# Kernel tuning notes

Hardware: AMD Instinct MI355X
Metric: run time of the kernel (lower is better)

The kernel has to match this reference:

```python
import jax, jax.numpy as jnp
import numpy as np

N, E, IN, HID, OUT = 50000, 800000, 128, 64, 32
ALPHA, BETA, DIVIDER = 0.5, 0.5, 5.0


def _gcn_conv(x, edge_index, W, b, alpha=ALPHA, beta=BETA):
    """DirectedGCNConv.forward: add self loops, linear, degree-normalized gather-mul-scatter."""
    n = x.shape[0]
    loops = jnp.arange(n, dtype=edge_index.dtype)
    row = jnp.concatenate([edge_index[0], loops])  # sources
    col = jnp.concatenate([edge_index[1], loops])  # targets
    x = x @ W.T + b                                # [n, out]
    ones = jnp.ones(row.shape[0], dtype=x.dtype)
    in_deg = jax.ops.segment_sum(ones, col, num_segments=n)
    out_deg = jax.ops.segment_sum(ones, row, num_segments=n)
    norm = in_deg[col] ** (-alpha) * out_deg[row] ** (-beta)  # [E+n]
    msgs = norm[:, None] * x[row]                  # gather + scale
    return jax.ops.segment_sum(msgs, col, num_segments=n)  # scatter-add aggr


def _source_enc(x, ei, W1, b1, W2, b2):
    x = jax.nn.relu(_gcn_conv(x, ei, W1, b1))
    return _gcn_conv(x, jnp.flip(ei, axis=0), W2, b2)


def _target_enc(x, ei, W1, b1, W2, b2):
    x = jax.nn.relu(_gcn_conv(x, jnp.flip(ei, axis=0), W1, b1))
    return _gcn_conv(x, ei, W2, b2)


def setup_inputs() -> dict:
    key = jax.random.key(0)
    ks = jax.random.split(key, 24)

    def lin(kw, kb, o, i, scale):
        return (jax.random.normal(kw, (o, i), jnp.float32) * scale,
                jax.random.normal(kb, (o,), jnp.float32) * 0.01)

    s1 = (2.0 / (IN + HID)) ** 0.5
    s2 = (2.0 / (HID + OUT)) ** 0.5
    inp = {
        "s": jax.random.normal(ks[0], (N, IN), jnp.float32),
        "t": jax.random.normal(ks[1], (N, IN), jnp.float32),
        "edge_index": jax.random.randint(ks[2], (2, E), 0, N, jnp.int32),
        "noise_s": jax.random.normal(ks[3], (N, OUT), jnp.float32),
        "noise_t": jax.random.normal(ks[4], (N, OUT), jnp.float32),
    }
    names = ["sm", "sl", "tm", "tl"]  # source/target mu/logstd encoders
    k = 5
    for nm in names:
        W1, b1 = lin(ks[k], ks[k + 1], HID, IN, s1); k += 2
        W2, b2 = lin(ks[k], ks[k + 1], OUT, HID, s2); k += 2
        inp[nm + "1_W"], inp[nm + "1_b"] = W1, b1
        inp[nm + "2_W"], inp[nm + "2_b"] = W2, b2
    return inp


def reference(s, t, edge_index, noise_s, noise_t,
              sm1_W, sm1_b, sm2_W, sm2_b,
              sl1_W, sl1_b, sl2_W, sl2_b,
              tm1_W, tm1_b, tm2_W, tm2_b,
              tl1_W, tl1_b, tl2_W, tl2_b):
    s_mu = _source_enc(s, edge_index, sm1_W, sm1_b, sm2_W, sm2_b)
    s_logstd = _source_enc(s, edge_index, sl1_W, sl1_b, sl2_W, sl2_b)
    t_mu = _target_enc(t, edge_index, tm1_W, tm1_b, tm2_W, tm2_b)
    t_logstd = _target_enc(t, edge_index, tl1_W, tl1_b, tl2_W, tl2_b)
    # reparametrize_edges (training mode), noise materialized as input
    s_out = s_mu + noise_s * jnp.exp(s_logstd) / DIVIDER
    t_out = t_mu + noise_t * jnp.exp(t_logstd) / DIVIDER
    return (s_out, t_out)
```

## Files before the change

### kernel.cpp

```cpp
#include <hip/hip_runtime.h>
#include <hip/hip_fp16.h>
#include <math.h>

#define N_NODES 50000
#define NPACK 25000
#define E_EDGES 800000
#define NCHUNKS ((N_NODES + 1023) / 1024)
#define LIN_BLOCKS 1564
#define QCH 64
#define CHUNK (E_EDGES / QCH)
#define CHUNK4 (CHUNK / 4)
#define OCT_NODES 12500
#define OCT_PACK 6250
#define HIST_BLOCKS 512
#define HL_GRID (HIST_BLOCKS + LIN_BLOCKS)
#define FOCT_NODES 6250
#define FOCT_PACK 3125
#define FILL_BLOCKS 1024
#define LCAP 4096

typedef _Float16 half8 __attribute__((ext_vector_type(8)));
typedef float f32x4 __attribute__((ext_vector_type(4)));

__device__ inline float fac_from(unsigned int u) {
    unsigned short us = (unsigned short)(u >> 16);
    __half h;
    __builtin_memcpy(&h, &us, 2);
    return __half2float(h);
}

__device__ inline int unpack_cnt(const unsigned int* cntp, int i) {
    unsigned int w = cntp[i >> 1];
    return (i & 1) ? (int)(w >> 16) : (int)(w & 0xffff);
}

__global__ __launch_bounds__(256) void w2h_kernel(const float* __restrict__ sW2a,
                                                  const float* __restrict__ sW2b,
                                                  const float* __restrict__ tW2a,
                                                  const float* __restrict__ tW2b,
                                                  const float* __restrict__ sW1a,
                                                  const float* __restrict__ sW1b,
                                                  const float* __restrict__ tW1a,
                                                  const float* __restrict__ tW1b,
                                                  __half* __restrict__ hw2,
                                                  __half* __restrict__ hw1) {
    int i = blockIdx.x * 256 + threadIdx.x;
    if (i < 4 * 2048) {
        const float* s2[4] = { sW2a, sW2b, tW2a, tW2b };
        hw2[i] = __float2half(s2[i >> 11][i & 2047]);
        return;
    }
    int j = i - 4 * 2048;
    if (j < 4 * 8192) {
        const float* s1[4] = { sW1a, sW1b, tW1a, tW1b };
        hw1[j] = __float2half(s1[j >> 13][j & 8191]);
    }
}

__global__ __launch_bounds__(256) void hist_lin1_kernel(const int* __restrict__ ei0,
                                                        const int* __restrict__ ei1,
                                                        unsigned int* __restrict__ ghist,
                                                        unsigned short* __restrict__ list,
                                                        unsigned int* __restrict__ cnt_bkt,
                                                        const float* __restrict__ Xs,
                                                        const float* __restrict__ Xt,
                                                        const __half* __restrict__ hw1,
                                                        const float* __restrict__ sba,
                                                        const float* __restrict__ sbb,
                                                        const float* __restrict__ tba,
                                                        const float* __restrict__ tbb,
                                                        __half* __restrict__ As,
                                                        __half* __restrict__ At, int n) {
    __shared__ unsigned int h[OCT_PACK];
    __shared__ unsigned int lcnt;
    int bx = blockIdx.x;
    int tid = threadIdx.x;
    if (bx < HIST_BLOCKS) {
        int oct = bx & 3, q = (bx >> 2) & 63, dir = bx >> 8;
        for (int i = tid; i < OCT_PACK; i += 256) h[i] = 0;
        if (tid == 0) lcnt = 0;
        __syncthreads();
        const int* key = dir ? ei0 : ei1;
        const uint4* key4 = (const uint4*)(key + q * CHUNK);
        unsigned short* lst = list + ((size_t)(dir * QCH + q) * 4 + oct) * LCAP;
        int lo = oct * OCT_NODES;
        for (int j = tid; j < CHUNK4; j += 256) {
            uint4 k4 = key4[j];
            int vv[4] = { (int)k4.x, (int)k4.y, (int)k4.z, (int)k4.w };
#pragma unroll
            for (int e = 0; e < 4; ++e) {
                unsigned int d = (unsigned int)(vv[e] - lo);
                if (d < OCT_NODES) {
                    atomicAdd(&h[d >> 1], 1u << ((d & 1) * 16));
                    unsigned int slot = atomicAdd(&lcnt, 1u);
                    if (slot < LCAP) lst[slot] = (unsigned short)(j * 4 + e);
                }
            }
        }
        __syncthreads();
        unsigned int* g = ghist + (size_t)(dir * QCH + q) * NPACK + oct * OCT_PACK;
        for (int i = tid; i < OCT_PACK; i += 256) g[i] = h[i];
        if (tid == 0) cnt_bkt[dir * 256 + q * 4 + oct] = (lcnt < LCAP) ? lcnt : LCAP;
        return;
    }
    int lidx = bx - HIST_BLOCKS;
    int y = lidx & 1;
    int xb = lidx >> 1;
    const float* X = y ? Xt : Xs;
    const __half* Wset[2] = { hw1 + (size_t)(y * 2 + 0) * 8192,
                              hw1 + (size_t)(y * 2 + 1) * 8192 };
    const float* bset[2] = { y ? tba : sba, y ? tbb : sbb };
    __half* A = y ? At : As;

    int w = tid >> 6, lane = tid & 63;
    int quad = lane >> 4, col = lane & 15;
    int node0 = xb * 64 + w * 16;

    half8 afrag[4];
    {
        int row = node0 + col;
        if (row >= n) row = n - 1;
        const float* xr = X + (size_t)row * 128 + quad * 8;
#pragma unroll
        for (int kc = 0; kc < 4; ++kc) {
            float4 f0 = *(const float4*)(xr + kc * 32);
            float4 f1 = *(const float4*)(xr + kc * 32 + 4);
            half8 hh;
            hh[0] = (_Float16)f0.x; hh[1] = (_Float16)f0.y;
            hh[2] = (_Float16)f0.z; hh[3] = (_Float16)f0.w;
            hh[4] = (_Float16)f1.x; hh[5] = (_Float16)f1.y;
            hh[6] = (_Float16)f1.z; hh[7] = (_Float16)f1.w;
            afrag[kc] = hh;
        }
    }

#pragma unroll
    for (int set = 0; set < 2; ++set) {
        const __half* Ws = Wset[set] + (size_t)0;
#pragma unroll
        for (int nt = 0; nt < 4; ++nt) {
            float bb = bset[set][nt * 16 + col];
            f32x4 acc = { bb, bb, bb, bb };
            const __half* wr = Ws + (size_t)(nt * 16 + col) * 128 + quad * 8;
#pragma unroll
            for (int kc = 0; kc < 4; ++kc) {
                half8 bfr = *(const half8*)(wr + kc * 32);
                acc = __builtin_amdgcn_mfma_f32_16x16x32_f16(afrag[kc], bfr, acc, 0, 0, 0);
            }
#pragma unroll
            for (int r = 0; r < 4; ++r) {
                int node = node0 + quad * 4 + r;
                if (node < n)
                    A[(size_t)node * 128 + set * 64 + nt * 16 + col] = __float2half(acc[r]);
            }
        }
    }
}

__global__ __launch_bounds__(256) void nodescan_kernel(unsigned int* __restrict__ ghist,
                                                       unsigned int* __restrict__ cntp) {
    int vp = blockIdx.x * 256 + threadIdx.x;
    int dir = blockIdx.y;
    if (vp >= NPACK) return;
    unsigned int lo = 0, hi = 0;
    unsigned int* g = ghist + (size_t)dir * QCH * NPACK + vp;
#pragma unroll 4
    for (int q = 0; q < QCH; ++q) {
        unsigned int w = g[(size_t)q * NPACK];
        g[(size_t)q * NPACK] = lo | (hi << 16);
        lo += w & 0xffff;
        hi += w >> 16;
    }
    cntp[dir * NPACK + vp] = lo | (hi << 16);
}

__global__ __launch_bounds__(1024) void scan_chunk2_kernel(const unsigned int* __restrict__ cntp,
                                                           int* __restrict__ offs_f,
                                                           int* __restrict__ offs_b,
                                                           int* __restrict__ part_f,
                                                           int* __restrict__ part_b, int n) {
    const unsigned int* cnt = cntp + (blockIdx.y ? NPACK : 0);
    int* offs = blockIdx.y ? offs_b : offs_f;
    int* partials = blockIdx.y ? part_b : part_f;
    __shared__ int sh[1024];
    int tid = threadIdx.x;
    int i = blockIdx.x * 1024 + tid;
    int v = (i < n) ? unpack_cnt(cnt, i) : 0;
    sh[tid] = v;
    __syncthreads();
    for (int off = 1; off < 1024; off <<= 1) {
        int add = (tid >= off) ? sh[tid - off] : 0;
        __syncthreads();
        sh[tid] += add;
        __syncthreads();
    }
    if (i < n) offs[i] = sh[tid] - v;
    if (tid == 1023) partials[blockIdx.x] = sh[tid];
}

__global__ __launch_bounds__(256) void addback_deg_kernel(int* __restrict__ offs_f,
                                                          int* __restrict__ offs_b,
                                                          const int* __restrict__ part_f,
                                                          const int* __restrict__ part_b,
                                                          const unsigned int* __restrict__ cntp,
                                                          float* dsi, float* dti,
                                                          unsigned short* __restrict__ h_dsi,
                                                          unsigned short* __restrict__ h_dti,
                                                          int n, int nchunks) {
    __shared__ int sp[64];
    int tid = threadIdx.x;
    const int* part = blockIdx.y ? part_b : part_f;
    if (tid < 64) sp[tid] = (tid < nchunks) ? part[tid] : 0;
    __syncthreads();
    if (tid == 0) {
        int run = 0;
        for (int k = 0; k < 64; ++k) { int t = sp[k]; sp[k] = run; run += t; }
    }
    __syncthreads();
    int i = blockIdx.x * 256 + tid;
    if (blockIdx.y == 0) {
        if (i < n) {
            offs_f[i] += sp[i >> 10];
            float f = rsqrtf((float)(unpack_cnt(cntp, i) + 1));
            dti[i] = f;
            __half hf = __float2half(f);
            unsigned short hb; __builtin_memcpy(&hb, &hf, 2);
            h_dti[i] = hb;
        } else if (i == n) offs_f[n] = sp[nchunks];
    } else {
        if (i < n) {
            offs_b[i] += sp[i >> 10];
            float f = rsqrtf((float)(unpack_cnt(cntp + NPACK, i) + 1));
            dsi[i] = f;
            __half hf = __float2half(f);
            unsigned short hb; __builtin_memcpy(&hb, &hf, 2);
            h_dsi[i] = hb;
        } else if (i == n) offs_b[n] = sp[nchunks];
    }
}

__global__ __launch_bounds__(256) void fill_kernel(const int* __restrict__ ei0,
                                                   const int* __restrict__ ei1,
                                                   const unsigned int* __restrict__ ghist,
                                                   const int* __restrict__ offs_f,
                                                   const int* __restrict__ offs_b,
                                                   const unsigned short* __restrict__ h_dsi,
                                                   const unsigned short* __restrict__ h_dti,
                                                   unsigned int* __restrict__ pay_f,
                                                   unsigned int* __restrict__ pay_b,
                                                   const unsigned short* __restrict__ list,
                                                   const unsigned int* __restrict__ cnt_bkt) {
    __shared__ unsigned int pos[FOCT_NODES];
    int bx = blockIdx.x;
    int foct = bx & 7, q = (bx >> 3) & 63, dir = bx >> 9;
    int oct = foct >> 1;
    int tid = threadIdx.x;
    const unsigned int* pref = ghist + (size_t)(dir * QCH + q) * NPACK + foct * FOCT_PACK;
    const int* offs = dir ? offs_b : offs_f;
    int lo = foct * FOCT_NODES;
    for (int d = tid; d < FOCT_NODES; d += 256) {
        unsigned int pw = pref[d >> 1];
        int cb = (d & 1) ? (int)(pw >> 16) : (int)(pw & 0xffff);
        pos[d] = (unsigned int)(offs[lo + d] + cb);
    }
    __syncthreads();
    const int* key = dir ? ei0 : ei1;
    const int* pid = dir ? ei1 : ei0;
    const unsigned short* hfac = dir ? h_dti : h_dsi;
    unsigned int* pay = dir ? pay_b : pay_f;
    const unsigned short* lst = list + ((size_t)(dir * QCH + q) * 4 + oct) * LCAP;
    int cnt = (int)cnt_bkt[dir * 256 + q * 4 + oct];
    int base = q * CHUNK;
    for (int j = tid; j < cnt; j += 256) {
        int gi = base + (int)lst[j];
        int v = key[gi];
        unsigned int d = (unsigned int)(v - lo);
        if (d < FOCT_NODES) {
            int id = pid[gi];
            unsigned int p = atomicAdd(&pos[d], 1u);
            unsigned int hb = hfac[id];
            pay[p] = (unsigned int)id | (hb << 16);
        }
    }
}

__device__ inline void acc_fma(float* acc, uint4 u, float f) {
    const __half2* h = (const __half2*)&u;
    float2 f0 = __half22float2(h[0]);
    float2 f1 = __half22float2(h[1]);
    float2 f2 = __half22float2(h[2]);
    float2 f3 = __half22float2(h[3]);
    acc[0] += f * f0.x; acc[1] += f * f0.y; acc[2] += f * f1.x; acc[3] += f * f1.y;
    acc[4] += f * f2.x; acc[5] += f * f2.y; acc[6] += f * f3.x; acc[7] += f * f3.y;
}

__global__ __launch_bounds__(256) void pull_lin2_kernel(const __half* __restrict__ As,
                                                        const __half* __restrict__ At,
                                                        __half* __restrict__ Cs,
                                                        __half* __restrict__ Ct,
                                                        const int* __restrict__ offs_f,
                                                        const int* __restrict__ offs_b,
                                                        const unsigned int* __restrict__ pay_f,
                                                        const unsigned int* __restrict__ pay_b,
                                                        const float* __restrict__ dsi,
                                                        const float* __restrict__ dti,
                                                        const float* __restrict__ sb2a,
                                                        const float* __restrict__ sb2b,
                                                        const float* __restrict__ tb2a,
                                                        const float* __restrict__ tb2b,
                                                        const __half* __restrict__ hw2, int n) {
    int y = blockIdx.y;
    const __half* xw = y ? At : As;
    __half* C = y ? Ct : Cs;
    const int* offs = y ? offs_b : offs_f;
    const unsigned int* pay = y ? pay_b : pay_f;
    const float* fac_self  = y ? dsi : dti;
    const float* fac_other = y ? dti : dsi;
    const float* b2a = y ? tb2a : sb2a;
    const float* b2b = y ? tb2b : sb2b;

    __shared__ __half xsh[16 * 136];

    int tid = threadIdx.x;
    int ln = tid >> 4;
    int f4 = tid & 15;
    int v = blockIdx.x * 16 + ln;
    int i = offs[v], end = offs[v + 1];
    const uint4* xw16 = (const uint4*)xw;

    float acc[8] = {0, 0, 0, 0, 0, 0, 0, 0};
    acc_fma(acc, xw16[v * 16 + f4], fac_other[v]);
    while (i < end && (i & 3)) {
        unsigned int pk = pay[i];
        acc_fma(acc, xw16[(pk & 0xffff) * 16 + f4], fac_from(pk));
        ++i;
    }
    for (; i + 3 < end; i += 4) {
        uint4 pk = *(const uint4*)(pay + i);
        int s0 = pk.x & 0xffff, s1 = pk.y & 0xffff;
        int s2 = pk.z & 0xffff, s3 = pk.w & 0xffff;
        uint4 ua = xw16[s0 * 16 + f4];
        uint4 ub = xw16[s1 * 16 + f4];
        uint4 uc = xw16[s2 * 16 + f4];
        uint4 ud = xw16[s3 * 16 + f4];
        acc_fma(acc, ua, fac_from(pk.x));
        acc_fma(acc, ub, fac_from(pk.y));
        acc_fma(acc, uc, fac_from(pk.z));
        acc_fma(acc, ud, fac_from(pk.w));
    }
    for (; i < end; ++i) {
        unsigned int pk = pay[i];
        acc_fma(acc, xw16[(pk & 0xffff) * 16 + f4], fac_from(pk));
    }

    float fs = fac_self[v];
    half8 hx;
#pragma unroll
    for (int j = 0; j < 8; ++j) hx[j] = (_Float16)fmaxf(acc[j] * fs, 0.0f);
    *(half8*)&xsh[ln * 136 + f4 * 8] = hx;
    __syncthreads();

    int w = tid >> 6, lane = tid & 63;
    int s = w >> 1, nt = w & 1;
    int quad = lane >> 4, col = lane & 15;
    float bb = (s ? b2b : b2a)[nt * 16 + col];
    f32x4 cacc = { bb, bb, bb, bb };
    const __half* hw = hw2 + (size_t)(y * 2 + s) * 2048;
#pragma unroll
    for (int t = 0; t < 2; ++t) {
        half8 af = *(const half8*)&xsh[col * 136 + s * 64 + t * 32 + quad * 8];
        half8 bf = *(const half8*)&hw[(nt * 16 + col) * 64 + t * 32 + quad * 8];
        cacc = __builtin_amdgcn_mfma_f32_16x16x32_f16(af, bf, cacc, 0, 0, 0);
    }
    int vbase = blockIdx.x * 16 + quad * 4;
    int o = s * 32 + nt * 16 + col;
#pragma unroll
    for (int r = 0; r < 4; ++r)
        C[(size_t)(vbase + r) * 64 + o] = __float2half(cacc[r]);
}

__global__ __launch_bounds__(256) void final_pull2_kernel(const __half* __restrict__ Cs,
                                                          const __half* __restrict__ Ct,
                                                          float* __restrict__ out_s,
                                                          float* __restrict__ out_t,
                                                          const int* __restrict__ offs_f,
                                                          const int* __restrict__ offs_b,
                                                          const unsigned int* __restrict__ pay_f,
                                                          const unsigned int* __restrict__ pay_b,
                                                          const float* __restrict__ dsi,
                                                          const float* __restrict__ dti,
                                                          const float* __restrict__ noise_s,
                                                          const float* __restrict__ noise_t,
                                                          int n) {
    int y = blockIdx.y;
    const __half* xw = y ? Ct : Cs;
    float* out = y ? out_t : out_s;
    const int* offs = y ? offs_f : offs_b;
    const unsigned int* pay = y ? pay_f : pay_b;
    const float* fac_self  = y ? dti : dsi;
    const float* fac_other = y ? dsi : dti;
    const float* noise = y ? noise_t : noise_s;

    const uint4* xw16 = (const uint4*)xw;
    int ln = threadIdx.x >> 3;
    int f4 = threadIdx.x & 7;
    int v = blockIdx.x * 32 + ln;
    if (v >= n) return;
    int i = offs[v], end = offs[v + 1];

    float acc[8] = {0, 0, 0, 0, 0, 0, 0, 0};
    acc_fma(acc, xw16[v * 8 + f4], fac_other[v]);
    while (i < end && (i & 3)) {
        unsigned int pk = pay[i];
        acc_fma(acc, xw16[(pk & 0xffff) * 8 + f4], fac_from(pk));
        ++i;
    }
    for (; i + 3 < end; i += 4) {
        uint4 pk = *(const uint4*)(pay + i);
        int s0 = pk.x & 0xffff, s1 = pk.y & 0xffff;
        int s2 = pk.z & 0xffff, s3 = pk.w & 0xffff;
        uint4 ua = xw16[s0 * 8 + f4];
        uint4 ub = xw16[s1 * 8 + f4];
        uint4 uc = xw16[s2 * 8 + f4];
        uint4 ud = xw16[s3 * 8 + f4];
        acc_fma(acc, ua, fac_from(pk.x));
        acc_fma(acc, ub, fac_from(pk.y));
        acc_fma(acc, uc, fac_from(pk.z));
        acc_fma(acc, ud, fac_from(pk.w));
    }
    for (; i < end; ++i) {
        unsigned int pk = pay[i];
        acc_fma(acc, xw16[(pk & 0xffff) * 8 + f4], fac_from(pk));
    }

    float fs = fac_self[v];
#pragma unroll
    for (int j = 0; j < 8; ++j) acc[j] *= fs;

    int lane = threadIdx.x & 63;
    float lg[8];
#pragma unroll
    for (int j = 0; j < 8; ++j) lg[j] = __shfl(acc[j], lane + 4);
    if (f4 < 4) {
        const float4* nz4 = (const float4*)noise;
        float4 n0 = nz4[v * 8 + f4 * 2];
        float4 n1 = nz4[v * 8 + f4 * 2 + 1];
        float4 r0, r1;
        r0.x = acc[0] + n0.x * expf(lg[0]) * 0.2f;
        r0.y = acc[1] + n0.y * expf(lg[1]) * 0.2f;
        r0.z = acc[2] + n0.z * expf(lg[2]) * 0.2f;
        r0.w = acc[3] + n0.w * expf(lg[3]) * 0.2f;
        r1.x = acc[4] + n1.x * expf(lg[4]) * 0.2f;
        r1.y = acc[5] + n1.y * expf(lg[5]) * 0.2f;
        r1.z = acc[6] + n1.z * expf(lg[6]) * 0.2f;
        r1.w = acc[7] + n1.w * expf(lg[7]) * 0.2f;
        float4* o4 = (float4*)out;
        o4[v * 8 + f4 * 2]     = r0;
        o4[v * 8 + f4 * 2 + 1] = r1;
    }
}

extern "C" void kernel_launch(void* const* d_in, const int* in_sizes, int n_in,
                              void* d_out, int out_size, void* d_ws, size_t ws_size,
                              hipStream_t stream) {
    const float* s       = (const float*)d_in[0];
    const float* t       = (const float*)d_in[1];
    const int*   ei      = (const int*)d_in[2];
    const float* noise_s = (const float*)d_in[3];
    const float* noise_t = (const float*)d_in[4];
    const float* sm1_W = (const float*)d_in[5];  const float* sm1_b = (const float*)d_in[6];
    const float* sm2_W = (const float*)d_in[7];  const float* sm2_b = (const float*)d_in[8];
    const float* sl1_W = (const float*)d_in[9];  const float* sl1_b = (const float*)d_in[10];
    const float* sl2_W = (const float*)d_in[11]; const float* sl2_b = (const float*)d_in[12];
    const float* tm1_W = (const float*)d_in[13]; const float* tm1_b = (const float*)d_in[14];
    const float* tm2_W = (const float*)d_in[15]; const float* tm2_b = (const float*)d_in[16];
    const float* tl1_W = (const float*)d_in[17]; const float* tl1_b = (const float*)d_in[18];
    const float* tl2_W = (const float*)d_in[19]; const float* tl2_b = (const float*)d_in[20];

    const int* ei0 = ei;
    const int* ei1 = ei + E_EDGES;

    __half* A_s = (__half*)d_ws;
    __half* A_t = A_s + (size_t)N_NODES * 128;
    __half* C_s = A_t + (size_t)N_NODES * 128;
    __half* C_t = C_s + (size_t)N_NODES * 64;
    unsigned int* pay_fwd = (unsigned int*)(C_t + (size_t)N_NODES * 64);
    unsigned int* pay_bwd = pay_fwd + E_EDGES;
    float* dsi = (float*)(pay_bwd + E_EDGES);
    float* dti = dsi + N_NODES;
    int* offs_fwd = (int*)(dti + N_NODES);
    int* offs_bwd = offs_fwd + N_NODES + 1;
    unsigned int* cntp = (unsigned int*)(offs_bwd + N_NODES + 1);
    int* part_fwd = (int*)(cntp + 2 * NPACK);
    int* part_bwd = part_fwd + NCHUNKS + 1;
    unsigned short* h_dsi = (unsigned short*)(part_bwd + NCHUNKS + 1);
    unsigned short* h_dti = h_dsi + N_NODES;
    unsigned short* list  = h_dti + N_NODES;
    unsigned int* cnt_bkt = (unsigned int*)(list + (size_t)HIST_BLOCKS * LCAP);
    __half* hw2 = (__half*)(((uintptr_t)(cnt_bkt + 512) + 15) & ~(uintptr_t)15);
    __half* hw1 = hw2 + 4 * 2048;

    unsigned int* ghist = (unsigned int*)C_s;

    float* s_out = (float*)d_out;
    float* t_out = (float*)d_out + N_NODES * 32;

    dim3 blk(256);
    dim3 agrid((N_NODES + 1 + 255) / 256, 2);
    dim3 pgrid(N_NODES / 16, 2);
    dim3 fgrid((N_NODES + 31) / 32, 2);
    dim3 nsgrid((NPACK + 255) / 256, 2);

    w2h_kernel<<<160, blk, 0, stream>>>(sm2_W, sl2_W, tm2_W, tl2_W,
                                        sm1_W, sl1_W, tm1_W, tl1_W, hw2, hw1);
    hist_lin1_kernel<<<HL_GRID, blk, 0, stream>>>(
        ei0, ei1, ghist, list, cnt_bkt,
        s, t, hw1, sm1_b, sl1_b, tm1_b, tl1_b,
        A_s, A_t, N_NODES);
    nodescan_kernel<<<nsgrid, blk, 0, stream>>>(ghist, cntp);
    scan_chunk2_kernel<<<dim3(NCHUNKS, 2), 1024, 0, stream>>>(
        cntp, offs_fwd, offs_bwd, part_fwd, part_bwd, N_NODES);
    addback_deg_kernel<<<agrid, blk, 0, stream>>>(offs_fwd, offs_bwd, part_fwd, part_bwd,
                                                  cntp, dsi, dti, h_dsi, h_dti,
                                                  N_NODES, NCHUNKS);
    fill_kernel<<<FILL_BLOCKS, blk, 0, stream>>>(ei0, ei1, ghist, offs_fwd, offs_bwd,
                                                 h_dsi, h_dti, pay_fwd, pay_bwd,
                                                 list, cnt_bkt);

    pull_lin2_kernel<<<pgrid, blk, 0, stream>>>(A_s, A_t, C_s, C_t,
                                                offs_fwd, offs_bwd, pay_fwd, pay_bwd,
                                                dsi, dti,
                                                sm2_b, sl2_b, tm2_b, tl2_b, hw2, N_NODES);
    final_pull2_kernel<<<fgrid, blk, 0, stream>>>(C_s, C_t, s_out, t_out,
                                                  offs_fwd, offs_bwd, pay_fwd, pay_bwd,
                                                  dsi, dti, noise_s, noise_t, N_NODES);
}
```

Before: 299.7 us.

## Fuse per-node histogram scan into chunk scan and unroll edge gathers by eight

```diff
diff --git a/kernel.cpp b/kernel.cpp
--- a/kernel.cpp
+++ b/kernel.cpp
@@ -27,11 +27,6 @@
     __half h;
     __builtin_memcpy(&h, &us, 2);
     return __half2float(h);
-}
-
-__device__ inline int unpack_cnt(const unsigned int* cntp, int i) {
-    unsigned int w = cntp[i >> 1];
-    return (i & 1) ? (int)(w >> 16) : (int)(w & 0xffff);
 }
 
 __global__ __launch_bounds__(256) void w2h_kernel(const float* __restrict__ sW2a,
@@ -136,7 +131,7 @@
 
 #pragma unroll
     for (int set = 0; set < 2; ++set) {
-        const __half* Ws = Wset[set] + (size_t)0;
+        const __half* Ws = Wset[set];
 #pragma unroll
         for (int nt = 0; nt < 4; ++nt) {
             float bb = bset[set][nt * 16 + col];
@@ -157,36 +152,56 @@
     }
 }
 
-__global__ __launch_bounds__(256) void nodescan_kernel(unsigned int* __restrict__ ghist,
-                                                       unsigned int* __restrict__ cntp) {
-    int vp = blockIdx.x * 256 + threadIdx.x;
+__global__ __launch_bounds__(1024) void scan_fused_kernel(unsigned int* __restrict__ ghist,
+                                                          int* __restrict__ offs_f,
+                                                          int* __restrict__ offs_b,
+                                                          int* __restrict__ part_f,
+                                                          int* __restrict__ part_b,
+                                                          float* __restrict__ dsi,
+                                                          float* __restrict__ dti,
+                                                          unsigned short* __restrict__ h_dsi,
+                                                          unsigned short* __restrict__ h_dti,
+                                                          int n) {
+    __shared__ int sh[1024];
     int dir = blockIdx.y;
-    if (vp >= NPACK) return;
-    unsigned int lo = 0, hi = 0;
-    unsigned int* g = ghist + (size_t)dir * QCH * NPACK + vp;
+    int bx = blockIdx.x;
+    int tid = threadIdx.x;
+    if (tid < 512) {
+        int vp = bx * 512 + tid;
+        unsigned int lo = 0, hi = 0;
+        if (vp < NPACK) {
+            unsigned int* g = ghist + (size_t)dir * QCH * NPACK + vp;
 #pragma unroll 4
-    for (int q = 0; q < QCH; ++q) {
-        unsigned int w = g[(size_t)q * NPACK];
-        g[(size_t)q * NPACK] = lo | (hi << 16);
-        lo += w & 0xffff;
-        hi += w >> 16;
-    }
-    cntp[dir * NPACK + vp] = lo | (hi << 16);
-}
-
-__global__ __launch_bounds__(1024) void scan_chunk2_kernel(const unsigned int* __restrict__ cntp,
-                                                           int* __restrict__ offs_f,
-                                                           int* __restrict__ offs_b,
-                                                           int* __restrict__ part_f,
-                                                           int* __restrict__ part_b, int n) {
-    const unsigned int* cnt = cntp + (blockIdx.y ? NPACK : 0);
-    int* offs = blockIdx.y ? offs_b : offs_f;
-    int* partials = blockIdx.y ? part_b : part_f;
-    __shared__ int sh[1024];
-    int tid = threadIdx.x;
-    int i = blockIdx.x * 1024 + tid;
-    int v = (i < n) ? unpack_cnt(cnt, i) : 0;
-    sh[tid] = v;
+            for (int q = 0; q < QCH; ++q) {
+                unsigned int w = g[(size_t)q * NPACK];
+                g[(size_t)q * NPACK] = lo | (hi << 16);
+                lo += w & 0xffff;
+                hi += w >> 16;
+            }
+            float f0 = rsqrtf((float)(lo + 1));
+            float f1 = rsqrtf((float)(hi + 1));
+            __half hf0 = __float2half(f0), hf1 = __float2half(f1);
+            unsigned short hb0, hb1;
+            __builtin_memcpy(&hb0, &hf0, 2);
+            __builtin_memcpy(&hb1, &hf1, 2);
+            int v0 = vp * 2, v1 = vp * 2 + 1;
+            if (dir == 0) {
+                dti[v0] = f0; dti[v1] = f1;
+                h_dti[v0] = hb0; h_dti[v1] = hb1;
+            } else {
+                dsi[v0] = f0; dsi[v1] = f1;
+                h_dsi[v0] = hb0; h_dsi[v1] = hb1;
+            }
+        }
+        sh[2 * tid]     = (int)lo;
+        sh[2 * tid + 1] = (int)hi;
+    }
+    __syncthreads();
+    int i = bx * 1024 + tid;
+    int v = sh[tid];
+    __syncthreads();
+    int run = v;
+    sh[tid] = run;
     __syncthreads();
     for (int off = 1; off < 1024; off <<= 1) {
         int add = (tid >= off) ? sh[tid - off] : 0;
@@ -194,22 +209,21 @@
         sh[tid] += add;
         __syncthreads();
     }
+    int* offs = dir ? offs_b : offs_f;
+    int* partials = dir ? part_b : part_f;
     if (i < n) offs[i] = sh[tid] - v;
-    if (tid == 1023) partials[blockIdx.x] = sh[tid];
-}
-
-__global__ __launch_bounds__(256) void addback_deg_kernel(int* __restrict__ offs_f,
-                                                          int* __restrict__ offs_b,
-                                                          const int* __restrict__ part_f,
-                                                          const int* __restrict__ part_b,
-                                                          const unsigned int* __restrict__ cntp,
-                                                          float* dsi, float* dti,
-                                                          unsigned short* __restrict__ h_dsi,
-                                                          unsigned short* __restrict__ h_dti,
-                                                          int n, int nchunks) {
+    if (tid == 1023) partials[bx] = sh[tid];
+}
+
+__global__ __launch_bounds__(256) void addback_kernel(int* __restrict__ offs_f,
+                                                      int* __restrict__ offs_b,
+                                                      const int* __restrict__ part_f,
+                                                      const int* __restrict__ part_b,
+                                                      int n, int nchunks) {
     __shared__ int sp[64];
     int tid = threadIdx.x;
     const int* part = blockIdx.y ? part_b : part_f;
+    int* offs = blockIdx.y ? offs_b : offs_f;
     if (tid < 64) sp[tid] = (tid < nchunks) ? part[tid] : 0;
     __syncthreads();
     if (tid == 0) {
@@ -218,25 +232,8 @@
     }
     __syncthreads();
     int i = blockIdx.x * 256 + tid;
-    if (blockIdx.y == 0) {
-        if (i < n) {
-            offs_f[i] += sp[i >> 10];
-            float f = rsqrtf((float)(unpack_cnt(cntp, i) + 1));
-            dti[i] = f;
-            __half hf = __float2half(f);
-            unsigned short hb; __builtin_memcpy(&hb, &hf, 2);
-            h_dti[i] = hb;
-        } else if (i == n) offs_f[n] = sp[nchunks];
-    } else {
-        if (i < n) {
-            offs_b[i] += sp[i >> 10];
-            float f = rsqrtf((float)(unpack_cnt(cntp + NPACK, i) + 1));
-            dsi[i] = f;
-            __half hf = __float2half(f);
-            unsigned short hb; __builtin_memcpy(&hb, &hf, 2);
-            h_dsi[i] = hb;
-        } else if (i == n) offs_b[n] = sp[nchunks];
-    }
+    if (i < n) offs[i] += sp[i >> 10];
+    else if (i == n) offs[n] = sp[nchunks];
 }
 
 __global__ __launch_bounds__(256) void fill_kernel(const int* __restrict__ ei0,
@@ -335,14 +332,32 @@
         acc_fma(acc, xw16[(pk & 0xffff) * 16 + f4], fac_from(pk));
         ++i;
     }
+    for (; i + 7 < end; i += 8) {
+        uint4 pk0 = *(const uint4*)(pay + i);
+        uint4 pk1 = *(const uint4*)(pay + i + 4);
+        uint4 ua = xw16[(pk0.x & 0xffff) * 16 + f4];
+        uint4 ub = xw16[(pk0.y & 0xffff) * 16 + f4];
+        uint4 uc = xw16[(pk0.z & 0xffff) * 16 + f4];
+        uint4 ud = xw16[(pk0.w & 0xffff) * 16 + f4];
+        uint4 ue = xw16[(pk1.x & 0xffff) * 16 + f4];
+        uint4 uf = xw16[(pk1.y & 0xffff) * 16 + f4];
+        uint4 ug = xw16[(pk1.z & 0xffff) * 16 + f4];
+        uint4 uh = xw16[(pk1.w & 0xffff) * 16 + f4];
+        acc_fma(acc, ua, fac_from(pk0.x));
+        acc_fma(acc, ub, fac_from(pk0.y));
+        acc_fma(acc, uc, fac_from(pk0.z));
+        acc_fma(acc, ud, fac_from(pk0.w));
+        acc_fma(acc, ue, fac_from(pk1.x));
+        acc_fma(acc, uf, fac_from(pk1.y));
+        acc_fma(acc, ug, fac_from(pk1.z));
+        acc_fma(acc, uh, fac_from(pk1.w));
+    }
     for (; i + 3 < end; i += 4) {
         uint4 pk = *(const uint4*)(pay + i);
-        int s0 = pk.x & 0xffff, s1 = pk.y & 0xffff;
-        int s2 = pk.z & 0xffff, s3 = pk.w & 0xffff;
-        uint4 ua = xw16[s0 * 16 + f4];
-        uint4 ub = xw16[s1 * 16 + f4];
-        uint4 uc = xw16[s2 * 16 + f4];
-        uint4 ud = xw16[s3 * 16 + f4];
+        uint4 ua = xw16[(pk.x & 0xffff) * 16 + f4];
+        uint4 ub = xw16[(pk.y & 0xffff) * 16 + f4];
+        uint4 uc = xw16[(pk.z & 0xffff) * 16 + f4];
+        uint4 ud = xw16[(pk.w & 0xffff) * 16 + f4];
         acc_fma(acc, ua, fac_from(pk.x));
         acc_fma(acc, ub, fac_from(pk.y));
         acc_fma(acc, uc, fac_from(pk.z));
@@ -415,14 +430,32 @@
         acc_fma(acc, xw16[(pk & 0xffff) * 8 + f4], fac_from(pk));
         ++i;
     }
+    for (; i + 7 < end; i += 8) {
+        uint4 pk0 = *(const uint4*)(pay + i);
+        uint4 pk1 = *(const uint4*)(pay + i + 4);
+        uint4 ua = xw16[(pk0.x & 0xffff) * 8 + f4];
+        uint4 ub = xw16[(pk0.y & 0xffff) * 8 + f4];
+        uint4 uc = xw16[(pk0.z & 0xffff) * 8 + f4];
+        uint4 ud = xw16[(pk0.w & 0xffff) * 8 + f4];
+        uint4 ue = xw16[(pk1.x & 0xffff) * 8 + f4];
+        uint4 uf = xw16[(pk1.y & 0xffff) * 8 + f4];
+        uint4 ug = xw16[(pk1.z & 0xffff) * 8 + f4];
+        uint4 uh = xw16[(pk1.w & 0xffff) * 8 + f4];
+        acc_fma(acc, ua, fac_from(pk0.x));
+        acc_fma(acc, ub, fac_from(pk0.y));
+        acc_fma(acc, uc, fac_from(pk0.z));
+        acc_fma(acc, ud, fac_from(pk0.w));
+        acc_fma(acc, ue, fac_from(pk1.x));
+        acc_fma(acc, uf, fac_from(pk1.y));
+        acc_fma(acc, ug, fac_from(pk1.z));
+        acc_fma(acc, uh, fac_from(pk1.w));
+    }
     for (; i + 3 < end; i += 4) {
         uint4 pk = *(const uint4*)(pay + i);
-        int s0 = pk.x & 0xffff, s1 = pk.y & 0xffff;
-        int s2 = pk.z & 0xffff, s3 = pk.w & 0xffff;
-        uint4 ua = xw16[s0 * 8 + f4];
-        uint4 ub = xw16[s1 * 8 + f4];
-        uint4 uc = xw16[s2 * 8 + f4];
-        uint4 ud = xw16[s3 * 8 + f4];
+        uint4 ua = xw16[(pk.x & 0xffff) * 8 + f4];
+        uint4 ub = xw16[(pk.y & 0xffff) * 8 + f4];
+        uint4 uc = xw16[(pk.z & 0xffff) * 8 + f4];
+        uint4 ud = xw16[(pk.w & 0xffff) * 8 + f4];
         acc_fma(acc, ua, fac_from(pk.x));
         acc_fma(acc, ub, fac_from(pk.y));
         acc_fma(acc, uc, fac_from(pk.z));
@@ -490,8 +523,7 @@
     float* dti = dsi + N_NODES;
     int* offs_fwd = (int*)(dti + N_NODES);
     int* offs_bwd = offs_fwd + N_NODES + 1;
-    unsigned int* cntp = (unsigned int*)(offs_bwd + N_NODES + 1);
-    int* part_fwd = (int*)(cntp + 2 * NPACK);
+    int* part_fwd = offs_bwd + N_NODES + 1;
     int* part_bwd = part_fwd + NCHUNKS + 1;
     unsigned short* h_dsi = (unsigned short*)(part_bwd + NCHUNKS + 1);
     unsigned short* h_dti = h_dsi + N_NODES;
@@ -509,7 +541,6 @@
     dim3 agrid((N_NODES + 1 + 255) / 256, 2);
     dim3 pgrid(N_NODES / 16, 2);
     dim3 fgrid((N_NODES + 31) / 32, 2);
-    dim3 nsgrid((NPACK + 255) / 256, 2);
 
     w2h_kernel<<<160, blk, 0, stream>>>(sm2_W, sl2_W, tm2_W, tl2_W,
                                         sm1_W, sl1_W, tm1_W, tl1_W, hw2, hw1);
@@ -517,12 +548,11 @@
         ei0, ei1, ghist, list, cnt_bkt,
         s, t, hw1, sm1_b, sl1_b, tm1_b, tl1_b,
         A_s, A_t, N_NODES);
-    nodescan_kernel<<<nsgrid, blk, 0, stream>>>(ghist, cntp);
-    scan_chunk2_kernel<<<dim3(NCHUNKS, 2), 1024, 0, stream>>>(
-        cntp, offs_fwd, offs_bwd, part_fwd, part_bwd, N_NODES);
-    addback_deg_kernel<<<agrid, blk, 0, stream>>>(offs_fwd, offs_bwd, part_fwd, part_bwd,
-                                                  cntp, dsi, dti, h_dsi, h_dti,
-                                                  N_NODES, NCHUNKS);
+    scan_fused_kernel<<<dim3(NCHUNKS, 2), 1024, 0, stream>>>(
+        ghist, offs_fwd, offs_bwd, part_fwd, part_bwd,
+        dsi, dti, h_dsi, h_dti, N_NODES);
+    addback_kernel<<<agrid, blk, 0, stream>>>(offs_fwd, offs_bwd, part_fwd, part_bwd,
+                                              N_NODES, NCHUNKS);
     fill_kernel<<<FILL_BLOCKS, blk, 0, stream>>>(ei0, ei1, ghist, offs_fwd, offs_bwd,
                                                  h_dsi, h_dti, pay_fwd, pay_bwd,
                                                  list, cnt_bkt);
```

Result: no change. 303.0 us (+1.1%).
